# Performance work log

Hardware: AMD Instinct MI355X
Metric: run time of the kernel (lower is better)

The kernel has to match this reference:

```python
import jax, jax.numpy as jnp
import numpy as np

N_EDGES = 20000
K_MAX = 16            # triplet slots per edge
N_TRIP = N_EDGES * K_MAX
EMB = 128             # emb_size
INTERM = 64           # emb_size_interm
NSPH = 7              # num_spherical
UNITS_OUT = 128


def setup_inputs() -> dict:
    key = jax.random.key(0)
    k1, k2, k3, k4 = jax.random.split(key, 4)
    rbf_W1 = jax.random.normal(k1, (N_EDGES, INTERM, NSPH), dtype=jnp.float32)
    sph = jax.random.normal(k2, (N_EDGES, NSPH, K_MAX), dtype=jnp.float32)
    m = jax.random.normal(k3, (N_TRIP, EMB), dtype=jnp.float32)
    # Consistent triplet->(edge, slot) mapping: every edge has exactly K_MAX triplets,
    # so (id_reduce, Kidx) pairs are unique and max(Kidx)+1 == K_MAX == sph.shape[2].
    id_reduce = jnp.repeat(jnp.arange(N_EDGES, dtype=jnp.int64), K_MAX)
    Kidx = jnp.tile(jnp.arange(K_MAX, dtype=jnp.int64), N_EDGES)
    # he_orthogonal_init approximated with scaled normal (statistics only affect init, not math)
    weight = jax.random.normal(k4, (EMB, INTERM, UNITS_OUT), dtype=jnp.float32) / np.sqrt(INTERM)
    return {"rbf_W1": rbf_W1, "sph": sph, "m": m, "weight": weight,
            "id_reduce": id_reduce, "Kidx": Kidx}


def reference(rbf_W1, sph, m, weight, id_reduce, Kidx):
    nEdges = rbf_W1.shape[0]
    Kmax = sph.shape[2]           # static; equals max(Kidx)+1 by construction
    emb_size = m.shape[1]
    # scatter triplet embeddings into dense (nEdges, Kmax, emb) tensor
    m2 = jnp.zeros((nEdges, Kmax, emb_size), dtype=m.dtype).at[id_reduce, Kidx].set(m)
    sum_k = jnp.matmul(sph, m2)            # (nEdges, nsph, emb)
    rbf_W1_sum_k = jnp.matmul(rbf_W1, sum_k)  # (nEdges, interm, emb)
    # fused bilinear + sum over emb axis: equals sum_e (rbf_W1_sum_k[:, :, e] @ weight[e])
    m_ca = jnp.einsum('nie,eio->no', rbf_W1_sum_k, weight)  # (nEdges, units_out)
    return m_ca
```

## Files before the change

kernel.cpp:

```cpp
#include <hip/hip_runtime.h>

#define NEDGES 20000
#define KMAX 16
#define NTRIP (NEDGES*KMAX)
#define EMB 128
#define INTERM 64
#define NSPH 7
#define UNITS 128
#define KSTEPS 256

typedef __attribute__((ext_vector_type(8))) short short8;
typedef __attribute__((ext_vector_type(4))) float floatx4;
typedef __attribute__((ext_vector_type(2))) float v2f;

__device__ __forceinline__ unsigned bf16pair(float a, float b) {
    unsigned ua = __float_as_uint(a), ub = __float_as_uint(b);
    ua = (ua + 0x7fffu + ((ua >> 16) & 1u)) >> 16;
    ub = (ub + 0x7fffu + ((ub >> 16) & 1u)) & 0xffff0000u;
    return ua | ub;
}
__device__ __forceinline__ unsigned short bf16rne(float a) {
    unsigned u = __float_as_uint(a);
    return (unsigned short)((u + 0x7fffu + ((u >> 16) & 1u)) >> 16);
}
__device__ __forceinline__ v2f splat2(float f) { v2f r; r.x = f; r.y = f; return r; }

__global__ __launch_bounds__(256)
void prep(const int* __restrict__ idr, const int* __restrict__ kix,
          int* __restrict__ inv, const float* __restrict__ w,
          uint4* __restrict__ w2f) {
    const int b = blockIdx.x, tid = threadIdx.x;
    if (b < NTRIP / 256) {
        int t = b * 256 + tid;
        int e = idr[t], k = kix[t];
        if ((unsigned)e < NEDGES && (unsigned)k < KMAX)
            inv[e * KMAX + k] = t;
    } else {
        int idx  = (b - NTRIP / 256) * 256 + tid;
        int lane = idx & 63;
        int ks   = (idx >> 6) & 255;
        int nt   = idx >> 14;
        int o  = nt * 16 + (lane & 15);
        int kb = ks * 32 + (lane >> 4) * 8;
        unsigned pk[4];
#pragma unroll
        for (int jj = 0; jj < 4; ++jj) {
            int k0 = kb + 2 * jj;
            int i0 = k0 >> 7, em0 = k0 & 127;
            int i1 = (k0 + 1) >> 7, em1 = (k0 + 1) & 127;
            float f0 = w[((size_t)em0 * INTERM + i0) * UNITS + o];
            float f1 = w[((size_t)em1 * INTERM + i1) * UNITS + o];
            pk[jj] = bf16pair(f0, f1);
        }
        w2f[idx] = make_uint4(pk[0], pk[1], pk[2], pk[3]);
    }
}

__global__ __launch_bounds__(512, 4)
void fused_all(const float* __restrict__ rbf, const float* __restrict__ sph,
               const float* __restrict__ m, const int* __restrict__ inv,
               const uint4* __restrict__ w2f, float* __restrict__ out) {
    __shared__ unsigned short rbf_s[32][528];
    __shared__ uint4 a_s[2][8 * 65];
    int*   inv_s = (int*)a_s;
    float* sph_s = (float*)((char*)a_s + 2048);

    const int tid = threadIdx.x;
    const size_t e0 = (size_t)blockIdx.x * 32;
    const int lane = tid & 63, wid = tid >> 6;
    const int e = tid >> 4, oct = tid & 15;
    const int mt = e >> 4;
    const int arow = mt * 4 + (oct >> 2);
    const int slot = (oct & 3) * 16 + (e & 15);

    floatx4 acc[2] = {{0.f, 0.f, 0.f, 0.f}, {0.f, 0.f, 0.f, 0.f}};
    uint4 wf[4];
    const uint4* wbase = w2f + ((size_t)wid * KSTEPS) * 64 + lane;
#pragma unroll
    for (int ksl = 0; ksl < 4; ++ksl) wf[ksl] = wbase[(size_t)ksl * 64];

    inv_s[tid] = inv[e0 * 16 + tid];
    for (int j = tid; j < 32 * 112; j += 512) sph_s[j] = sph[e0 * 112 + j];
    {
        const float4* rg = (const float4*)(rbf + e0 * 448);
        for (int f = tid; f < 3584; f += 512) {
            int ee = f / 112, idx = f - ee * 112;
            float4 v = rg[f];
            float vv[4] = {v.x, v.y, v.z, v.w};
            int rr = idx * 4;
#pragma unroll
            for (int x = 0; x < 4; ++x) {
                int r2 = rr + x, i = r2 / 7, s = r2 - i * 7;
                rbf_s[ee][i * 8 + s] = bf16rne(vv[x]);
            }
        }
    }
    __syncthreads();

    v2f skf[NSPH][4];
#pragma unroll
    for (int s = 0; s < NSPH; ++s)
#pragma unroll
        for (int h = 0; h < 4; ++h) skf[s][h] = splat2(0.f);
    {
        const float4* mrow = (const float4*)m;
        const int* ip = inv_s + e * 16;
        const float* sp = sph_s + e * 112;
#pragma unroll 2
        for (int k = 0; k < 16; ++k) {
            int t = ip[k];
            float4 v0 = make_float4(0.f, 0.f, 0.f, 0.f);
            float4 v1 = make_float4(0.f, 0.f, 0.f, 0.f);
            if ((unsigned)t < (unsigned)NTRIP) {
                const float4* tp = mrow + (size_t)t * 32 + oct * 2;
                v0 = tp[0];
                v1 = tp[1];
            }
            v2f mv[4];
            mv[0].x = v0.x; mv[0].y = v0.y;
            mv[1].x = v0.z; mv[1].y = v0.w;
            mv[2].x = v1.x; mv[2].y = v1.y;
            mv[3].x = v1.z; mv[3].y = v1.w;
#pragma unroll
            for (int s = 0; s < NSPH; ++s) {
                float cs = sp[s * 16 + k];
#pragma unroll
                for (int h = 0; h < 4; ++h)
                    skf[s][h] = __builtin_elementwise_fma(splat2(cs), mv[h], skf[s][h]);
            }
        }
    }
    __syncthreads();

    auto buildChunk = [&](int i, uint4* dst) {
        uint4 r4 = *(const uint4*)&rbf_s[e][i * 8];
        float rv[NSPH];
        rv[0] = __uint_as_float(r4.x << 16);
        rv[1] = __uint_as_float(r4.x & 0xffff0000u);
        rv[2] = __uint_as_float(r4.y << 16);
        rv[3] = __uint_as_float(r4.y & 0xffff0000u);
        rv[4] = __uint_as_float(r4.z << 16);
        rv[5] = __uint_as_float(r4.z & 0xffff0000u);
        rv[6] = __uint_as_float(r4.w << 16);
        v2f v[4];
#pragma unroll
        for (int h = 0; h < 4; ++h) v[h] = splat2(rv[0]) * skf[0][h];
#pragma unroll
        for (int s = 1; s < NSPH; ++s)
#pragma unroll
            for (int h = 0; h < 4; ++h)
                v[h] = __builtin_elementwise_fma(splat2(rv[s]), skf[s][h], v[h]);
        dst[arow * 65 + slot] = make_uint4(bf16pair(v[0].x, v[0].y), bf16pair(v[1].x, v[1].y),
                                           bf16pair(v[2].x, v[2].y), bf16pair(v[3].x, v[3].y));
    };

    buildChunk(0, a_s[0]);
    __syncthreads();

    for (int c = 0; c < 64; ++c) {
        const int cur = c & 1, nxt = cur ^ 1;
        if (c < 63) buildChunk(c + 1, a_s[nxt]);
#pragma unroll
        for (int ksl = 0; ksl < 4; ++ksl) {
            short8 a0 = __builtin_bit_cast(short8, a_s[cur][ksl * 65 + lane]);
            short8 a1 = __builtin_bit_cast(short8, a_s[cur][(4 + ksl) * 65 + lane]);
            short8 b  = __builtin_bit_cast(short8, wf[ksl]);
            acc[0] = __builtin_amdgcn_mfma_f32_16x16x32_bf16(a0, b, acc[0], 0, 0, 0);
            acc[1] = __builtin_amdgcn_mfma_f32_16x16x32_bf16(a1, b, acc[1], 0, 0, 0);
        }
        const int kn = (c < 63 ? c + 1 : 63) * 4;
#pragma unroll
        for (int ksl = 0; ksl < 4; ++ksl) wf[ksl] = wbase[(size_t)(kn + ksl) * 64];
        __syncthreads();
    }

    const int col = lane & 15, r0 = (lane >> 4) * 4;
#pragma unroll
    for (int h = 0; h < 2; ++h) {
        size_t ebase = e0 + (size_t)h * 16 + r0;
#pragma unroll
        for (int r = 0; r < 4; ++r)
            out[(ebase + r) * UNITS + wid * 16 + col] = acc[h][r];
    }
}

extern "C" void kernel_launch(void* const* d_in, const int* in_sizes, int n_in,
                              void* d_out, int out_size, void* d_ws, size_t ws_size,
                              hipStream_t stream) {
    const float* rbf = (const float*)d_in[0];
    const float* sph = (const float*)d_in[1];
    const float* m   = (const float*)d_in[2];
    const float* w   = (const float*)d_in[3];
    const int*   idr = (const int*)d_in[4];
    const int*   kix = (const int*)d_in[5];
    float* out = (float*)d_out;

    int*   inv = (int*)d_ws;
    uint4* w2f = (uint4*)((char*)d_ws + 0x140000);

    prep<<<NTRIP / 256 + 512, 256, 0, stream>>>(idr, kix, inv, w, w2f);
    fused_all<<<NEDGES / 32, 512, 0, stream>>>(rbf, sph, m, inv, w2f, out);
}
```

Measured before the change: 370.3 us.

## Precompute padded bf16 rbf in prep, prefetch m rows, swizzle A-tile LDS layout

Moves the fp32-to-bf16 conversion and 7-to-8 padding of rbf_W1 into the prep kernel. The fused kernel then streams one 16-byte rbf vector per chunk straight from global memory into registers, and the 33 KB rbf staging array leaves shared memory, which may allow more blocks per CU. The m gather loop is software-pipelined with a 4-deep register prefetch, and the A-tile LDS writes and reads use an XOR-style swizzle to cut bank conflicts. In exchange there is an extra global round trip for the padded rbf buffer and a longer prep kernel.

```diff
diff --git a/kernel.cpp b/kernel.cpp
--- a/kernel.cpp
+++ b/kernel.cpp
@@ -9,6 +9,10 @@
 #define UNITS 128
 #define KSTEPS 256
 
+#define SC_BLOCKS (NTRIP/256)
+#define W_BLOCKS  512
+#define RP_BLOCKS (NEDGES/4)
+
 typedef __attribute__((ext_vector_type(8))) short short8;
 typedef __attribute__((ext_vector_type(4))) float floatx4;
 typedef __attribute__((ext_vector_type(2))) float v2f;
@@ -19,24 +23,26 @@
     ub = (ub + 0x7fffu + ((ub >> 16) & 1u)) & 0xffff0000u;
     return ua | ub;
 }
-__device__ __forceinline__ unsigned short bf16rne(float a) {
-    unsigned u = __float_as_uint(a);
-    return (unsigned short)((u + 0x7fffu + ((u >> 16) & 1u)) >> 16);
-}
 __device__ __forceinline__ v2f splat2(float f) { v2f r; r.x = f; r.y = f; return r; }
+
+__device__ __forceinline__ int aunit(int row, int koct) {
+    int y = row >> 1;
+    return y * 8 + ((4 * (koct & 1) + (koct >> 1) + y + 2 * (row & 1)) & 7);
+}
 
 __global__ __launch_bounds__(256)
 void prep(const int* __restrict__ idr, const int* __restrict__ kix,
           int* __restrict__ inv, const float* __restrict__ w,
-          uint4* __restrict__ w2f) {
+          uint4* __restrict__ w2f, const float* __restrict__ rbf,
+          uint4* __restrict__ rpad) {
     const int b = blockIdx.x, tid = threadIdx.x;
-    if (b < NTRIP / 256) {
+    if (b < SC_BLOCKS) {
         int t = b * 256 + tid;
         int e = idr[t], k = kix[t];
         if ((unsigned)e < NEDGES && (unsigned)k < KMAX)
             inv[e * KMAX + k] = t;
-    } else {
-        int idx  = (b - NTRIP / 256) * 256 + tid;
+    } else if (b < SC_BLOCKS + W_BLOCKS) {
+        int idx  = (b - SC_BLOCKS) * 256 + tid;
         int lane = idx & 63;
         int ks   = (idx >> 6) & 255;
         int nt   = idx >> 14;
@@ -53,15 +59,22 @@
             pk[jj] = bf16pair(f0, f1);
         }
         w2f[idx] = make_uint4(pk[0], pk[1], pk[2], pk[3]);
+    } else {
+        int rb = b - (SC_BLOCKS + W_BLOCKS);
+        int e = rb * 4 + (tid >> 6), i = tid & 63;
+        const float* rs = rbf + (size_t)e * 448 + i * 7;
+        float s0 = rs[0], s1 = rs[1], s2 = rs[2], s3 = rs[3];
+        float s4 = rs[4], s5 = rs[5], s6 = rs[6];
+        rpad[(size_t)e * 64 + i] = make_uint4(bf16pair(s0, s1), bf16pair(s2, s3),
+                                              bf16pair(s4, s5), bf16pair(s6, 0.f));
     }
 }
 
 __global__ __launch_bounds__(512, 4)
-void fused_all(const float* __restrict__ rbf, const float* __restrict__ sph,
-               const float* __restrict__ m, const int* __restrict__ inv,
-               const uint4* __restrict__ w2f, float* __restrict__ out) {
-    __shared__ unsigned short rbf_s[32][528];
-    __shared__ uint4 a_s[2][8 * 65];
+void fused_all(const float* __restrict__ sph, const float* __restrict__ m,
+               const int* __restrict__ inv, const uint4* __restrict__ w2f,
+               const uint4* __restrict__ rpad, float* __restrict__ out) {
+    __shared__ uint4 a_s[2][520];
     int*   inv_s = (int*)a_s;
     float* sph_s = (float*)((char*)a_s + 2048);
 
@@ -69,32 +82,12 @@
     const size_t e0 = (size_t)blockIdx.x * 32;
     const int lane = tid & 63, wid = tid >> 6;
     const int e = tid >> 4, oct = tid & 15;
-    const int mt = e >> 4;
-    const int arow = mt * 4 + (oct >> 2);
-    const int slot = (oct & 3) * 16 + (e & 15);
-
-    floatx4 acc[2] = {{0.f, 0.f, 0.f, 0.f}, {0.f, 0.f, 0.f, 0.f}};
-    uint4 wf[4];
-    const uint4* wbase = w2f + ((size_t)wid * KSTEPS) * 64 + lane;
-#pragma unroll
-    for (int ksl = 0; ksl < 4; ++ksl) wf[ksl] = wbase[(size_t)ksl * 64];
+
+    const int wua = ((e >> 4) * 4 + (oct >> 2)) * 65 + aunit(e & 15, oct & 3);
+    const int runit = aunit(lane & 15, lane >> 4);
 
     inv_s[tid] = inv[e0 * 16 + tid];
     for (int j = tid; j < 32 * 112; j += 512) sph_s[j] = sph[e0 * 112 + j];
-    {
-        const float4* rg = (const float4*)(rbf + e0 * 448);
-        for (int f = tid; f < 3584; f += 512) {
-            int ee = f / 112, idx = f - ee * 112;
-            float4 v = rg[f];
-            float vv[4] = {v.x, v.y, v.z, v.w};
-            int rr = idx * 4;
-#pragma unroll
-            for (int x = 0; x < 4; ++x) {
-                int r2 = rr + x, i = r2 / 7, s = r2 - i * 7;
-                rbf_s[ee][i * 8 + s] = bf16rne(vv[x]);
-            }
-        }
-    }
     __syncthreads();
 
     v2f skf[NSPH][4];
@@ -106,15 +99,31 @@
         const float4* mrow = (const float4*)m;
         const int* ip = inv_s + e * 16;
         const float* sp = sph_s + e * 112;
-#pragma unroll 2
-        for (int k = 0; k < 16; ++k) {
+        float4 pb[4][2];
+#pragma unroll
+        for (int k = 0; k < 4; ++k) {
             int t = ip[k];
-            float4 v0 = make_float4(0.f, 0.f, 0.f, 0.f);
-            float4 v1 = make_float4(0.f, 0.f, 0.f, 0.f);
+            pb[k][0] = make_float4(0.f, 0.f, 0.f, 0.f);
+            pb[k][1] = make_float4(0.f, 0.f, 0.f, 0.f);
             if ((unsigned)t < (unsigned)NTRIP) {
                 const float4* tp = mrow + (size_t)t * 32 + oct * 2;
-                v0 = tp[0];
-                v1 = tp[1];
+                pb[k][0] = tp[0];
+                pb[k][1] = tp[1];
+            }
+        }
+#pragma unroll
+        for (int k = 0; k < 16; ++k) {
+            const int sl = k & 3;
+            float4 v0 = pb[sl][0], v1 = pb[sl][1];
+            if (k < 12) {
+                int t = ip[k + 4];
+                pb[sl][0] = make_float4(0.f, 0.f, 0.f, 0.f);
+                pb[sl][1] = make_float4(0.f, 0.f, 0.f, 0.f);
+                if ((unsigned)t < (unsigned)NTRIP) {
+                    const float4* tp = mrow + (size_t)t * 32 + oct * 2;
+                    pb[sl][0] = tp[0];
+                    pb[sl][1] = tp[1];
+                }
             }
             v2f mv[4];
             mv[0].x = v0.x; mv[0].y = v0.y;
@@ -130,18 +139,24 @@
             }
         }
     }
-    __syncthreads();
-
-    auto buildChunk = [&](int i, uint4* dst) {
-        uint4 r4 = *(const uint4*)&rbf_s[e][i * 8];
+
+    floatx4 acc[2] = {{0.f, 0.f, 0.f, 0.f}, {0.f, 0.f, 0.f, 0.f}};
+    uint4 wf[4];
+    const uint4* wbase = w2f + ((size_t)wid * KSTEPS) * 64 + lane;
+#pragma unroll
+    for (int ksl = 0; ksl < 4; ++ksl) wf[ksl] = wbase[(size_t)ksl * 64];
+    const uint4* rp_g = rpad + (e0 + e) * 64;
+    uint4 rpA = rp_g[0], rpB = rp_g[1];
+
+    auto buildChunk = [&](const uint4 rv4, uint4* dstbuf) {
         float rv[NSPH];
-        rv[0] = __uint_as_float(r4.x << 16);
-        rv[1] = __uint_as_float(r4.x & 0xffff0000u);
-        rv[2] = __uint_as_float(r4.y << 16);
-        rv[3] = __uint_as_float(r4.y & 0xffff0000u);
-        rv[4] = __uint_as_float(r4.z << 16);
-        rv[5] = __uint_as_float(r4.z & 0xffff0000u);
-        rv[6] = __uint_as_float(r4.w << 16);
+        rv[0] = __uint_as_float(rv4.x << 16);
+        rv[1] = __uint_as_float(rv4.x & 0xffff0000u);
+        rv[2] = __uint_as_float(rv4.y << 16);
+        rv[3] = __uint_as_float(rv4.y & 0xffff0000u);
+        rv[4] = __uint_as_float(rv4.z << 16);
+        rv[5] = __uint_as_float(rv4.z & 0xffff0000u);
+        rv[6] = __uint_as_float(rv4.w << 16);
         v2f v[4];
 #pragma unroll
         for (int h = 0; h < 4; ++h) v[h] = splat2(rv[0]) * skf[0][h];
@@ -150,28 +165,40 @@
 #pragma unroll
             for (int h = 0; h < 4; ++h)
                 v[h] = __builtin_elementwise_fma(splat2(rv[s]), skf[s][h], v[h]);
-        dst[arow * 65 + slot] = make_uint4(bf16pair(v[0].x, v[0].y), bf16pair(v[1].x, v[1].y),
-                                           bf16pair(v[2].x, v[2].y), bf16pair(v[3].x, v[3].y));
+        dstbuf[wua] = make_uint4(bf16pair(v[0].x, v[0].y), bf16pair(v[1].x, v[1].y),
+                                 bf16pair(v[2].x, v[2].y), bf16pair(v[3].x, v[3].y));
     };
 
-    buildChunk(0, a_s[0]);
     __syncthreads();
-
-    for (int c = 0; c < 64; ++c) {
+    buildChunk(rpA, a_s[0]);
+    rpA = rp_g[2];
+    __syncthreads();
+
+    auto body = [&](int c, uint4& rpSlot) {
         const int cur = c & 1, nxt = cur ^ 1;
-        if (c < 63) buildChunk(c + 1, a_s[nxt]);
+        if (c < 63) {
+            buildChunk(rpSlot, a_s[nxt]);
+            if (c < 61) rpSlot = rp_g[c + 3];
+        }
 #pragma unroll
         for (int ksl = 0; ksl < 4; ++ksl) {
-            short8 a0 = __builtin_bit_cast(short8, a_s[cur][ksl * 65 + lane]);
-            short8 a1 = __builtin_bit_cast(short8, a_s[cur][(4 + ksl) * 65 + lane]);
-            short8 b  = __builtin_bit_cast(short8, wf[ksl]);
-            acc[0] = __builtin_amdgcn_mfma_f32_16x16x32_bf16(a0, b, acc[0], 0, 0, 0);
-            acc[1] = __builtin_amdgcn_mfma_f32_16x16x32_bf16(a1, b, acc[1], 0, 0, 0);
-        }
-        const int kn = (c < 63 ? c + 1 : 63) * 4;
-#pragma unroll
-        for (int ksl = 0; ksl < 4; ++ksl) wf[ksl] = wbase[(size_t)(kn + ksl) * 64];
+            short8 a0 = __builtin_bit_cast(short8, a_s[cur][ksl * 65 + runit]);
+            short8 a1 = __builtin_bit_cast(short8, a_s[cur][(4 + ksl) * 65 + runit]);
+            short8 bb = __builtin_bit_cast(short8, wf[ksl]);
+            acc[0] = __builtin_amdgcn_mfma_f32_16x16x32_bf16(a0, bb, acc[0], 0, 0, 0);
+            acc[1] = __builtin_amdgcn_mfma_f32_16x16x32_bf16(a1, bb, acc[1], 0, 0, 0);
+        }
         __syncthreads();
+        if (c < 63) {
+#pragma unroll
+            for (int ksl = 0; ksl < 4; ++ksl)
+                wf[ksl] = wbase[(size_t)((c + 1) * 4 + ksl) * 64];
+        }
+    };
+
+    for (int c = 0; c < 64; c += 2) {
+        body(c, rpB);
+        body(c + 1, rpA);
     }
 
     const int col = lane & 15, r0 = (lane >> 4) * 4;
@@ -195,9 +222,10 @@
     const int*   kix = (const int*)d_in[5];
     float* out = (float*)d_out;
 
-    int*   inv = (int*)d_ws;
-    uint4* w2f = (uint4*)((char*)d_ws + 0x140000);
-
-    prep<<<NTRIP / 256 + 512, 256, 0, stream>>>(idr, kix, inv, w, w2f);
-    fused_all<<<NEDGES / 32, 512, 0, stream>>>(rbf, sph, m, inv, w2f, out);
-}
+    int*   inv  = (int*)d_ws;
+    uint4* w2f  = (uint4*)((char*)d_ws + 0x140000);
+    uint4* rpad = (uint4*)((char*)d_ws + 0x340000);
+
+    prep<<<SC_BLOCKS + W_BLOCKS + RP_BLOCKS, 256, 0, stream>>>(idr, kix, inv, w, w2f, rbf, rpad);
+    fused_all<<<NEDGES / 32, 512, 0, stream>>>(sph, m, inv, w2f, rpad, out);
+}
```

After: 467.7 us. +26.3%, slower.
